# Performance work log

Measured on AMD Instinct MI355X. Metric: run time of the kernel, lower is better.

The kernel has to match this reference:

```python
import jax, jax.numpy as jnp
import numpy as np

N = 100000
E = 1600000
IN = 770
H = 64
R = 3

def _w(key, shape):
    fan_in = shape[-2] if len(shape) >= 2 else shape[-1]
    return jax.random.normal(key, shape, dtype=jnp.float32) / np.sqrt(fan_in)

def setup_inputs() -> dict:
    key = jax.random.key(0)
    ks = jax.random.split(key, 24)
    x = jax.random.normal(ks[0], (N, IN), dtype=jnp.float32)
    edge_index = jax.random.randint(ks[1], (2, E), 0, N, dtype=jnp.int64)
    edge_type = jax.random.randint(ks[2], (E,), 0, R, dtype=jnp.int64)
    return {
        "x": x, "edge_index": edge_index, "edge_type": edge_type,
        "W1": _w(ks[3], (R, IN, H)), "root1": _w(ks[4], (IN, H)), "b1": jnp.zeros((H,), jnp.float32),
        "W2": _w(ks[5], (R, H, H)), "root2": _w(ks[6], (H, H)), "b2": jnp.zeros((H,), jnp.float32),
        "W3": _w(ks[7], (R, H, H)), "root3": _w(ks[8], (H, H)), "b3": jnp.zeros((H,), jnp.float32),
        "nw1": _w(ks[9], (H, H // 2)), "nb1": jnp.zeros((H // 2,), jnp.float32),
        "nw2": _w(ks[10], (H // 2, 2)), "nb2": jnp.zeros((2,), jnp.float32),
        "ew1": _w(ks[11], (2 * H, H)), "eb1": jnp.zeros((H,), jnp.float32),
        "ew2": _w(ks[12], (H, H // 2)), "eb2": jnp.zeros((H // 2,), jnp.float32),
        "ew3": _w(ks[13], (H // 2, 3)), "eb3": jnp.zeros((3,), jnp.float32),
    }

def rgcn_layer(x, W, root, b, src, dst, etype):
    # PyG RGCNConv (aggr='mean'): out = x@root + b + sum_r mean_r(x_src)@W_r
    out = x @ root + b
    msg = x[src]                       # [E, F] gather
    for r in range(R):
        m = (etype == r).astype(x.dtype)
        agg = jax.ops.segment_sum(msg * m[:, None], dst, num_segments=N)  # [N, F]
        cnt = jax.ops.segment_sum(m, dst, num_segments=N)                 # [N]
        out = out + (agg / jnp.maximum(cnt, 1.0)[:, None]) @ W[r]
    return out

def reference(x, edge_index, edge_type,
              W1, root1, b1, W2, root2, b2, W3, root3, b3,
              nw1, nb1, nw2, nb2, ew1, eb1, ew2, eb2, ew3, eb3):
    src, dst = edge_index[0], edge_index[1]
    x1 = jax.nn.relu(rgcn_layer(x, W1, root1, b1, src, dst, edge_type))
    x2 = jax.nn.relu(rgcn_layer(x1, W2, root2, b2, src, dst, edge_type))
    x3 = rgcn_layer(x2, W3, root3, b3, src, dst, edge_type) + x1
    node_out = jax.nn.relu(x3 @ nw1 + nb1) @ nw2 + nb2
    ef = jnp.concatenate([x3[src], x3[dst]], axis=-1)   # [E, 2H]
    h = jax.nn.relu(ef @ ew1 + eb1)
    h = jax.nn.relu(h @ ew2 + eb2)
    edge_out = h @ ew3 + eb3
    return node_out, edge_out
```

## Files before the change

kernel.cpp:

```cpp
#include <hip/hip_runtime.h>

typedef unsigned int uint;
typedef unsigned short ushort;
typedef short short8 __attribute__((ext_vector_type(8)));
typedef float f32x4 __attribute__((ext_vector_type(4)));
typedef float float4u __attribute__((ext_vector_type(4), aligned(4)));

#define MN 100000
#define ME 1600000
#define KIN 770

__device__ __forceinline__ ushort f2bf(float f) {
    union { float f; uint u; } c; c.f = f;
    uint r = (c.u + 0x7fffu + ((c.u >> 16) & 1u)) >> 16;
    return (ushort)r;
}
__device__ __forceinline__ float bf2f(ushort h) {
    union { uint u; float f; } c; c.u = ((uint)h) << 16;
    return c.f;
}
__device__ __forceinline__ float bflo(uint w) {
    union { uint u; float f; } c; c.u = w << 16; return c.f;
}
__device__ __forceinline__ float bfhi(uint w) {
    union { uint u; float f; } c; c.u = w & 0xffff0000u; return c.f;
}

__global__ void k_deg(const int* __restrict__ dstv, int* __restrict__ deg, int E) {
    int e = blockIdx.x * blockDim.x + threadIdx.x;
    if (e < E) atomicAdd(&deg[dstv[e]], 1);
}

__global__ void k_scan1(const int* __restrict__ deg, int* __restrict__ excl,
                        int* __restrict__ csums, int n) {
    __shared__ int a[256], b[256];
    int tid = threadIdx.x;
    int g = blockIdx.x * 256 + tid;
    int v = (g < n) ? deg[g] : 0;
    int *cur = a, *nxt = b;
    cur[tid] = v;
    __syncthreads();
    for (int off = 1; off < 256; off <<= 1) {
        int t = cur[tid];
        if (tid >= off) t += cur[tid - off];
        nxt[tid] = t;
        __syncthreads();
        int* tmp = cur; cur = nxt; nxt = tmp;
    }
    int inc = cur[tid];
    if (g < n) excl[g] = inc - v;
    if (tid == 255) csums[blockIdx.x] = inc;
}

__global__ void k_scan2(int* __restrict__ csums, int nchunks) {
    __shared__ int a[512], b[512];
    int tid = threadIdx.x;
    int v = (tid < nchunks) ? csums[tid] : 0;
    int *cur = a, *nxt = b;
    cur[tid] = v;
    __syncthreads();
    for (int off = 1; off < 512; off <<= 1) {
        int t = cur[tid];
        if (tid >= off) t += cur[tid - off];
        nxt[tid] = t;
        __syncthreads();
        int* tmp = cur; cur = nxt; nxt = tmp;
    }
    int inc = cur[tid];
    if (tid < nchunks) csums[tid] = inc - v;
}

__global__ void k_scan3(int* __restrict__ row_ptr, const int* __restrict__ csums,
                        int* __restrict__ cursor, int n, int E) {
    int g = blockIdx.x * blockDim.x + threadIdx.x;
    if (g < n) {
        int v = row_ptr[g] + csums[g >> 8];
        row_ptr[g] = v;
        cursor[g] = v;
    }
    if (g == n) row_ptr[n] = E;
}

__global__ void k_fill(const int* __restrict__ srcv, const int* __restrict__ dstv,
                       const int* __restrict__ et, int* __restrict__ cursor,
                       int* __restrict__ esrt, int* __restrict__ dstp,
                       int* __restrict__ eid, int E) {
    int e = blockIdx.x * blockDim.x + threadIdx.x;
    if (e < E) {
        int d = dstv[e];
        int pos = atomicAdd(&cursor[d], 1);
        esrt[pos] = srcv[e] | (et[e] << 17);
        dstp[pos] = d;
        eid[pos] = e;
    }
}

__global__ void k_pack_bt(const float* __restrict__ root, const float* __restrict__ W,
                          ushort* __restrict__ out, int K, int Kp) {
    int idx = blockIdx.x * blockDim.x + threadIdx.x;
    if (idx >= 256 * Kp) return;
    int j = idx / Kp, k = idx - j * Kp;
    float v = 0.f;
    if (k < K) {
        if (j < 64) v = root[k * 64 + j];
        else {
            int r = (j >> 6) - 1, jj = j & 63;
            v = W[((size_t)r * K + k) * 64 + jj];
        }
    }
    out[idx] = f2bf(v);
}

__global__ void k_packwab_bt(const float* __restrict__ ew1, ushort* __restrict__ out) {
    int idx = blockIdx.x * blockDim.x + threadIdx.x;
    if (idx >= 128 * 64) return;
    int j = idx >> 6, k = idx & 63;
    float v = (j < 64) ? ew1[k * 64 + j] : ew1[(64 + k) * 64 + (j - 64)];
    out[idx] = f2bf(v);
}

template<bool AFP32, int BN>
__global__ __launch_bounds__(512) void k_mm(const void* __restrict__ Ain,
                                            const ushort* __restrict__ BT,
                                            ushort* __restrict__ C,
                                            int M, int K, int Kp, int Nc) {
    constexpr int WN = BN / 4;
    constexpr int NF = WN / 16;
    constexpr int NBS = (4 * BN) / 512;
    __shared__ uint4 lds4[512 + 4 * BN];
    int tid = threadIdx.x;
    int lane = tid & 63, wid = tid >> 6;
    int l15 = lane & 15, kq = lane >> 4;
    int wm = wid >> 2, wn = wid & 3;
    int m0 = blockIdx.x * 128;
    int n0 = blockIdx.y * BN;

    int s_kp = tid >> 7;
    int s_row = tid & 127;
    int gm = m0 + s_row; if (gm > M - 1) gm = M - 1;

    const float*  Af = (const float*)Ain;
    const ushort* Ab = (const ushort*)Ain;

    f32x4 acc[4][NF];
    #pragma unroll
    for (int m = 0; m < 4; ++m)
        #pragma unroll
        for (int n = 0; n < NF; ++n)
            acc[m][n] = (f32x4)0.f;

    int nkt = (K + 31) >> 5;
    uint4 stA, stB[NBS];

    auto loadA = [&](int kt) {
        int k0 = kt << 5;
        int kb = k0 + s_kp * 8;
        if constexpr (AFP32) {
            const float* ap = Af + (size_t)gm * K + kb;
            float v[8];
            if (k0 + 32 <= K) {
                *(float4u*)&v[0] = *(const float4u*)ap;
                *(float4u*)&v[4] = *(const float4u*)(ap + 4);
            } else {
                #pragma unroll
                for (int i = 0; i < 8; ++i)
                    v[i] = (kb + i < K) ? ap[i] : 0.f;
            }
            uint w[4];
            #pragma unroll
            for (int i = 0; i < 4; ++i)
                w[i] = (uint)f2bf(v[2 * i]) | ((uint)f2bf(v[2 * i + 1]) << 16);
            stA = make_uint4(w[0], w[1], w[2], w[3]);
        } else {
            stA = *(const uint4*)(Ab + (size_t)gm * K + kb);
        }
    };
    auto loadB = [&](int kt) {
        int k0 = kt << 5;
        #pragma unroll
        for (int is = 0; is < NBS; ++is) {
            int slot = is * 512 + tid;
            int kp = slot / BN;
            int col = slot & (BN - 1);
            stB[is] = *(const uint4*)(BT + (size_t)(n0 + col) * Kp + k0 + kp * 8);
        }
    };

    loadA(0); loadB(0);
    for (int kt = 0; kt < nkt; ++kt) {
        __syncthreads();
        lds4[tid] = stA;
        #pragma unroll
        for (int is = 0; is < NBS; ++is)
            lds4[512 + is * 512 + tid] = stB[is];
        __syncthreads();
        if (kt + 1 < nkt) { loadA(kt + 1); loadB(kt + 1); }
        const short8* Asv = (const short8*)lds4;
        const short8* Bsv = (const short8*)(lds4 + 512);
        short8 a[4], b[NF];
        #pragma unroll
        for (int m = 0; m < 4; ++m)
            a[m] = Asv[kq * 128 + wm * 64 + m * 16 + l15];
        #pragma unroll
        for (int n = 0; n < NF; ++n)
            b[n] = Bsv[kq * BN + wn * WN + n * 16 + l15];
        #pragma unroll
        for (int m = 0; m < 4; ++m)
            #pragma unroll
            for (int n = 0; n < NF; ++n)
                acc[m][n] = __builtin_amdgcn_mfma_f32_16x16x32_bf16(a[m], b[n], acc[m][n], 0, 0, 0);
    }

    #pragma unroll
    for (int m = 0; m < 4; ++m) {
        int rbase = m0 + wm * 64 + m * 16 + kq * 4;
        #pragma unroll
        for (int n = 0; n < NF; ++n) {
            int col = n0 + wn * WN + n * 16 + l15;
            #pragma unroll
            for (int rg = 0; rg < 4; ++rg) {
                int r = rbase + rg;
                if (r < M) C[(size_t)r * Nc + col] = f2bf(acc[m][n][rg]);
            }
        }
    }
}

__global__ __launch_bounds__(256) void k_agg(const ushort* __restrict__ Y,
                                             const int* __restrict__ row_ptr,
                                             const int* __restrict__ esrt,
                                             const float* __restrict__ bias,
                                             const ushort* __restrict__ resid,
                                             ushort* __restrict__ Xout,
                                             int do_relu, int n) {
    int wid = (blockIdx.x * blockDim.x + threadIdx.x) >> 6;
    int lane = threadIdx.x & 63;
    if (wid >= n) return;
    int beg = row_ptr[wid], end = row_ptr[wid + 1];
    float self = bf2f(Y[(size_t)wid * 256 + lane]);
    float bv = bias[lane];
    float a0 = 0.f, a1 = 0.f, a2 = 0.f;
    int c0 = 0, c1 = 0, c2 = 0;
    int e = beg;
    for (; e + 4 <= end; e += 4) {
        int p0 = esrt[e], p1 = esrt[e + 1], p2 = esrt[e + 2], p3 = esrt[e + 3];
        float v0 = bf2f(Y[(size_t)(p0 & 0x1FFFF) * 256 + 64 + ((p0 >> 17) << 6) + lane]);
        float v1 = bf2f(Y[(size_t)(p1 & 0x1FFFF) * 256 + 64 + ((p1 >> 17) << 6) + lane]);
        float v2 = bf2f(Y[(size_t)(p2 & 0x1FFFF) * 256 + 64 + ((p2 >> 17) << 6) + lane]);
        float v3 = bf2f(Y[(size_t)(p3 & 0x1FFFF) * 256 + 64 + ((p3 >> 17) << 6) + lane]);
        int r0 = p0 >> 17, r1 = p1 >> 17, r2 = p2 >> 17, r3 = p3 >> 17;
        if (r0 == 0) { a0 += v0; c0++; } else if (r0 == 1) { a1 += v0; c1++; } else { a2 += v0; c2++; }
        if (r1 == 0) { a0 += v1; c0++; } else if (r1 == 1) { a1 += v1; c1++; } else { a2 += v1; c2++; }
        if (r2 == 0) { a0 += v2; c0++; } else if (r2 == 1) { a1 += v2; c1++; } else { a2 += v2; c2++; }
        if (r3 == 0) { a0 += v3; c0++; } else if (r3 == 1) { a1 += v3; c1++; } else { a2 += v3; c2++; }
    }
    for (; e < end; ++e) {
        int p = esrt[e];
        int r = p >> 17;
        float v = bf2f(Y[(size_t)(p & 0x1FFFF) * 256 + 64 + (r << 6) + lane]);
        if (r == 0) { a0 += v; c0++; } else if (r == 1) { a1 += v; c1++; } else { a2 += v; c2++; }
    }
    float res = self + bv;
    if (c0) res += a0 / (float)c0;
    if (c1) res += a1 / (float)c1;
    if (c2) res += a2 / (float)c2;
    if (do_relu) res = fmaxf(res, 0.f);
    if (resid) res += bf2f(resid[(size_t)wid * 64 + lane]);
    Xout[(size_t)wid * 64 + lane] = f2bf(res);
}

__global__ __launch_bounds__(256) void k_nodehead(const ushort* __restrict__ X3,
                                                  const float* __restrict__ nw1,
                                                  const float* __restrict__ nb1,
                                                  const float* __restrict__ nw2,
                                                  const float* __restrict__ nb2,
                                                  float* __restrict__ out, int n) {
    __shared__ float w1[64 * 32];
    __shared__ float w2[32 * 2];
    __shared__ float b1s[32];
    __shared__ float b2s[2];
    int tid = threadIdx.x;
    for (int i = tid; i < 64 * 32; i += 256) w1[i] = nw1[i];
    for (int i = tid; i < 32 * 2; i += 256) w2[i] = nw2[i];
    if (tid < 32) b1s[tid] = nb1[tid];
    if (tid < 2) b2s[tid] = nb2[tid];
    __syncthreads();
    int g = blockIdx.x * blockDim.x + tid;
    if (g >= n) return;
    float x[64];
    const uint4* xr = (const uint4*)(X3 + (size_t)g * 64);
    #pragma unroll
    for (int q = 0; q < 8; ++q) {
        uint4 u = xr[q];
        x[q * 8 + 0] = bflo(u.x); x[q * 8 + 1] = bfhi(u.x);
        x[q * 8 + 2] = bflo(u.y); x[q * 8 + 3] = bfhi(u.y);
        x[q * 8 + 4] = bflo(u.z); x[q * 8 + 5] = bfhi(u.z);
        x[q * 8 + 6] = bflo(u.w); x[q * 8 + 7] = bfhi(u.w);
    }
    float o0 = b2s[0], o1 = b2s[1];
    for (int j = 0; j < 32; ++j) {
        float h = b1s[j];
        #pragma unroll
        for (int k = 0; k < 64; ++k) h += x[k] * w1[k * 32 + j];
        h = fmaxf(h, 0.f);
        o0 += h * w2[j * 2 + 0];
        o1 += h * w2[j * 2 + 1];
    }
    out[g * 2 + 0] = o0;
    out[g * 2 + 1] = o1;
}

__global__ __launch_bounds__(256) void k_edgehead(const ushort* __restrict__ AB,
                                                  const int* __restrict__ esrt,
                                                  const int* __restrict__ dstp,
                                                  const int* __restrict__ eid,
                                                  const float* __restrict__ eb1,
                                                  const float* __restrict__ ew2,
                                                  const float* __restrict__ eb2,
                                                  const float* __restrict__ ew3,
                                                  const float* __restrict__ eb3,
                                                  float* __restrict__ out, int E) {
    __shared__ float w2[64 * 32];
    __shared__ float w3[32 * 3];
    __shared__ float b1s[64];
    __shared__ float b2s[32];
    __shared__ float b3s[3];
    int tid = threadIdx.x;
    for (int i = tid; i < 64 * 32; i += 256) w2[i] = ew2[i];
    for (int i = tid; i < 32 * 3; i += 256) w3[i] = ew3[i];
    if (tid < 64) b1s[tid] = eb1[tid];
    if (tid < 32) b2s[tid] = eb2[tid];
    if (tid < 3) b3s[tid] = eb3[tid];
    __syncthreads();
    int p = blockIdx.x * blockDim.x + tid;
    if (p >= E) return;
    int s = esrt[p] & 0x1FFFF;
    int d = dstp[p];
    int e = eid[p];
    const uint4* Ar = (const uint4*)(AB + (size_t)s * 128);
    uint4 a4[8];
    #pragma unroll
    for (int q = 0; q < 8; ++q) a4[q] = Ar[q];
    const uint4* Br = (const uint4*)(AB + (size_t)d * 128 + 64);
    float h2[32];
    #pragma unroll
    for (int j = 0; j < 32; ++j) h2[j] = 0.f;
    #pragma unroll
    for (int q = 0; q < 8; ++q) {
        uint4 ua = a4[q], ub = Br[q];
        float af[8], bfv[8];
        af[0] = bflo(ua.x); af[1] = bfhi(ua.x); af[2] = bflo(ua.y); af[3] = bfhi(ua.y);
        af[4] = bflo(ua.z); af[5] = bfhi(ua.z); af[6] = bflo(ua.w); af[7] = bfhi(ua.w);
        bfv[0] = bflo(ub.x); bfv[1] = bfhi(ub.x); bfv[2] = bflo(ub.y); bfv[3] = bfhi(ub.y);
        bfv[4] = bflo(ub.z); bfv[5] = bfhi(ub.z); bfv[6] = bflo(ub.w); bfv[7] = bfhi(ub.w);
        #pragma unroll
        for (int t = 0; t < 8; ++t) {
            int k = q * 8 + t;
            float h1 = fmaxf(af[t] + bfv[t] + b1s[k], 0.f);
            #pragma unroll
            for (int j = 0; j < 32; ++j) h2[j] += h1 * w2[k * 32 + j];
        }
    }
    float o0 = b3s[0], o1 = b3s[1], o2 = b3s[2];
    #pragma unroll
    for (int j = 0; j < 32; ++j) {
        float hh = fmaxf(h2[j] + b2s[j], 0.f);
        o0 += hh * w3[j * 3 + 0];
        o1 += hh * w3[j * 3 + 1];
        o2 += hh * w3[j * 3 + 2];
    }
    out[200000 + (size_t)e * 3 + 0] = o0;
    out[200000 + (size_t)e * 3 + 1] = o1;
    out[200000 + (size_t)e * 3 + 2] = o2;
}

extern "C" void kernel_launch(void* const* d_in, const int* in_sizes, int n_in,
                              void* d_out, int out_size, void* d_ws, size_t ws_size,
                              hipStream_t stream) {
    const float* x     = (const float*)d_in[0];
    const int*   ei    = (const int*)d_in[1];
    const int*   et    = (const int*)d_in[2];
    const float* W1    = (const float*)d_in[3];
    const float* root1 = (const float*)d_in[4];
    const float* b1    = (const float*)d_in[5];
    const float* W2    = (const float*)d_in[6];
    const float* root2 = (const float*)d_in[7];
    const float* b2    = (const float*)d_in[8];
    const float* W3    = (const float*)d_in[9];
    const float* root3 = (const float*)d_in[10];
    const float* b3    = (const float*)d_in[11];
    const float* nw1   = (const float*)d_in[12];
    const float* nb1   = (const float*)d_in[13];
    const float* nw2   = (const float*)d_in[14];
    const float* nb2   = (const float*)d_in[15];
    const float* ew1   = (const float*)d_in[16];
    const float* eb1   = (const float*)d_in[17];
    const float* ew2   = (const float*)d_in[18];
    const float* eb2   = (const float*)d_in[19];
    const float* ew3   = (const float*)d_in[20];
    const float* eb3   = (const float*)d_in[21];
    float* out = (float*)d_out;

    const int N = MN, E = ME;
    const int* srcv = ei;
    const int* dstv = ei + E;

    char* w = (char*)d_ws;
    ushort* Yb   = (ushort*)w; w += (size_t)N * 256 * 2;
    ushort* X1b  = (ushort*)w; w += (size_t)N * 64 * 2;
    ushort* X2b  = (ushort*)w; w += (size_t)N * 64 * 2;
    ushort* X3b  = (ushort*)w; w += (size_t)N * 64 * 2;
    ushort* ABb  = (ushort*)w; w += (size_t)N * 128 * 2;
    ushort* BT1  = (ushort*)w; w += 256 * 800 * 2;
    ushort* BT2  = (ushort*)w; w += 256 * 64 * 2;
    ushort* BT3  = (ushort*)w; w += 256 * 64 * 2;
    ushort* BTab = (ushort*)w; w += 128 * 64 * 2;
    int* deg     = (int*)w; w += (size_t)N * 4;
    int* row_ptr = (int*)w; w += (size_t)(N + 1) * 4;
    int* cursor  = (int*)w; w += (size_t)N * 4;
    int* esrt    = (int*)w; w += (size_t)E * 4;
    int* dstp    = (int*)w; w += (size_t)E * 4;
    int* eid     = (int*)w; w += (size_t)E * 4;
    int* csums   = (int*)w; w += 512 * 4;

    hipMemsetAsync(deg, 0, N * sizeof(int), stream);
    k_deg<<<(E + 255) / 256, 256, 0, stream>>>(dstv, deg, E);
    int nchunks = (N + 255) / 256;
    k_scan1<<<nchunks, 256, 0, stream>>>(deg, row_ptr, csums, N);
    k_scan2<<<1, 512, 0, stream>>>(csums, nchunks);
    k_scan3<<<(N + 256) / 256, 256, 0, stream>>>(row_ptr, csums, cursor, N, E);
    k_fill<<<(E + 255) / 256, 256, 0, stream>>>(srcv, dstv, et, cursor, esrt, dstp, eid, E);

    k_pack_bt<<<(256 * 800 + 255) / 256, 256, 0, stream>>>(root1, W1, BT1, KIN, 800);
    k_pack_bt<<<(256 * 64 + 255) / 256, 256, 0, stream>>>(root2, W2, BT2, 64, 64);
    k_pack_bt<<<(256 * 64 + 255) / 256, 256, 0, stream>>>(root3, W3, BT3, 64, 64);
    k_packwab_bt<<<(128 * 64 + 255) / 256, 256, 0, stream>>>(ew1, BTab);

    int gx = (N + 127) / 128;
    int agg_grid = (N * 64 + 255) / 256;

    k_mm<true, 256><<<dim3(gx, 1), 512, 0, stream>>>(x, BT1, Yb, N, KIN, 800, 256);
    k_agg<<<agg_grid, 256, 0, stream>>>(Yb, row_ptr, esrt, b1, nullptr, X1b, 1, N);

    k_mm<false, 256><<<dim3(gx, 1), 512, 0, stream>>>(X1b, BT2, Yb, N, 64, 64, 256);
    k_agg<<<agg_grid, 256, 0, stream>>>(Yb, row_ptr, esrt, b2, nullptr, X2b, 1, N);

    k_mm<false, 256><<<dim3(gx, 1), 512, 0, stream>>>(X2b, BT3, Yb, N, 64, 64, 256);
    k_agg<<<agg_grid, 256, 0, stream>>>(Yb, row_ptr, esrt, b3, X1b, X3b, 0, N);

    k_nodehead<<<(N + 255) / 256, 256, 0, stream>>>(X3b, nw1, nb1, nw2, nb2, out, N);

    k_mm<false, 128><<<dim3(gx, 1), 512, 0, stream>>>(X3b, BTab, ABb, N, 64, 64, 128);
    k_edgehead<<<(E + 255) / 256, 256, 0, stream>>>(ABb, esrt, dstp, eid, eb1, ew2, eb2, ew3, eb3, out, E);
}
```

Before: 1.244 ms.

## Double K-tile depth to 64 and coalesce A/B staging loads in GEMM

The GEMM kernel now processes a K-tile of 64 instead of 32 per iteration, staging two MFMA K-halves per LDS fill and halving the number of barrier pairs. Global loads are remapped so eight consecutive threads read one row's 64-element K span contiguously, improving coalescing for the fp32 input and the B matrix. The fp32-to-bf16 conversion is deferred until the LDS store, so loads of the next tile can be issued before conversion. The cost is doubled LDS use and more staging registers, and the padded B layout for layer 1 grows to 832 columns.

```diff
diff --git a/kernel.cpp b/kernel.cpp
--- a/kernel.cpp
+++ b/kernel.cpp
@@ -126,18 +126,18 @@
                                             int M, int K, int Kp, int Nc) {
     constexpr int WN = BN / 4;
     constexpr int NF = WN / 16;
-    constexpr int NBS = (4 * BN) / 512;
-    __shared__ uint4 lds4[512 + 4 * BN];
+    constexpr int BR = BN / 64;
+    __shared__ uint4 lds4[1024 + 8 * BN];
     int tid = threadIdx.x;
     int lane = tid & 63, wid = tid >> 6;
-    int l15 = lane & 15, kq = lane >> 4;
+    int l15 = lane & 15, kqw = lane >> 4;
     int wm = wid >> 2, wn = wid & 3;
     int m0 = blockIdx.x * 128;
     int n0 = blockIdx.y * BN;
 
-    int s_kp = tid >> 7;
-    int s_row = tid & 127;
-    int gm = m0 + s_row; if (gm > M - 1) gm = M - 1;
+    int s_g = tid & 7;
+    int s_h = s_g >> 2, s_kq = s_g & 3;
+    int s_r = tid >> 3;
 
     const float*  Af = (const float*)Ain;
     const ushort* Ab = (const ushort*)Ain;
@@ -149,71 +149,85 @@
         for (int n = 0; n < NF; ++n)
             acc[m][n] = (f32x4)0.f;
 
-    int nkt = (K + 31) >> 5;
-    uint4 stA, stB[NBS];
+    int nkt = (K + 63) >> 6;
+    float stAf[2][8];
+    uint4 stAb[2];
+    uint4 stB[BR];
 
     auto loadA = [&](int kt) {
-        int k0 = kt << 5;
-        int kb = k0 + s_kp * 8;
-        if constexpr (AFP32) {
-            const float* ap = Af + (size_t)gm * K + kb;
-            float v[8];
-            if (k0 + 32 <= K) {
-                *(float4u*)&v[0] = *(const float4u*)ap;
-                *(float4u*)&v[4] = *(const float4u*)(ap + 4);
+        int k0 = kt << 6;
+        int kb = k0 + s_g * 8;
+        #pragma unroll
+        for (int r = 0; r < 2; ++r) {
+            int gm = m0 + s_r + (r << 6);
+            if (gm > M - 1) gm = M - 1;
+            if constexpr (AFP32) {
+                const float* ap = Af + (size_t)gm * K + kb;
+                if (k0 + 64 <= K) {
+                    *(float4u*)&stAf[r][0] = *(const float4u*)ap;
+                    *(float4u*)&stAf[r][4] = *(const float4u*)(ap + 4);
+                } else {
+                    #pragma unroll
+                    for (int i = 0; i < 8; ++i)
+                        stAf[r][i] = (kb + i < K) ? ap[i] : 0.f;
+                }
             } else {
-                #pragma unroll
-                for (int i = 0; i < 8; ++i)
-                    v[i] = (kb + i < K) ? ap[i] : 0.f;
+                stAb[r] = *(const uint4*)(Ab + (size_t)gm * K + kb);
             }
-            uint w[4];
-            #pragma unroll
-            for (int i = 0; i < 4; ++i)
-                w[i] = (uint)f2bf(v[2 * i]) | ((uint)f2bf(v[2 * i + 1]) << 16);
-            stA = make_uint4(w[0], w[1], w[2], w[3]);
-        } else {
-            stA = *(const uint4*)(Ab + (size_t)gm * K + kb);
         }
     };
     auto loadB = [&](int kt) {
-        int k0 = kt << 5;
-        #pragma unroll
-        for (int is = 0; is < NBS; ++is) {
-            int slot = is * 512 + tid;
-            int kp = slot / BN;
-            int col = slot & (BN - 1);
-            stB[is] = *(const uint4*)(BT + (size_t)(n0 + col) * Kp + k0 + kp * 8);
+        int k0 = kt << 6;
+        #pragma unroll
+        for (int r = 0; r < BR; ++r) {
+            int col = s_r + (r << 6);
+            stB[r] = *(const uint4*)(BT + (size_t)(n0 + col) * Kp + k0 + s_g * 8);
         }
     };
 
     loadA(0); loadB(0);
     for (int kt = 0; kt < nkt; ++kt) {
         __syncthreads();
-        lds4[tid] = stA;
-        #pragma unroll
-        for (int is = 0; is < NBS; ++is)
-            lds4[512 + is * 512 + tid] = stB[is];
+        #pragma unroll
+        for (int r = 0; r < 2; ++r) {
+            uint4 val;
+            if constexpr (AFP32) {
+                uint w0 = (uint)f2bf(stAf[r][0]) | ((uint)f2bf(stAf[r][1]) << 16);
+                uint w1 = (uint)f2bf(stAf[r][2]) | ((uint)f2bf(stAf[r][3]) << 16);
+                uint w2 = (uint)f2bf(stAf[r][4]) | ((uint)f2bf(stAf[r][5]) << 16);
+                uint w3 = (uint)f2bf(stAf[r][6]) | ((uint)f2bf(stAf[r][7]) << 16);
+                val = make_uint4(w0, w1, w2, w3);
+            } else {
+                val = stAb[r];
+            }
+            lds4[s_h * 512 + s_kq * 128 + s_r + (r << 6)] = val;
+        }
+        #pragma unroll
+        for (int r = 0; r < BR; ++r)
+            lds4[1024 + s_h * (4 * BN) + s_kq * BN + s_r + (r << 6)] = stB[r];
         __syncthreads();
         if (kt + 1 < nkt) { loadA(kt + 1); loadB(kt + 1); }
         const short8* Asv = (const short8*)lds4;
-        const short8* Bsv = (const short8*)(lds4 + 512);
-        short8 a[4], b[NF];
-        #pragma unroll
-        for (int m = 0; m < 4; ++m)
-            a[m] = Asv[kq * 128 + wm * 64 + m * 16 + l15];
-        #pragma unroll
-        for (int n = 0; n < NF; ++n)
-            b[n] = Bsv[kq * BN + wn * WN + n * 16 + l15];
-        #pragma unroll
-        for (int m = 0; m < 4; ++m)
+        #pragma unroll
+        for (int h = 0; h < 2; ++h) {
+            short8 a[4], b[NF];
+            #pragma unroll
+            for (int m = 0; m < 4; ++m)
+                a[m] = Asv[h * 512 + kqw * 128 + wm * 64 + m * 16 + l15];
             #pragma unroll
             for (int n = 0; n < NF; ++n)
-                acc[m][n] = __builtin_amdgcn_mfma_f32_16x16x32_bf16(a[m], b[n], acc[m][n], 0, 0, 0);
+                b[n] = Asv[1024 + h * (4 * BN) + kqw * BN + wn * WN + n * 16 + l15];
+            #pragma unroll
+            for (int m = 0; m < 4; ++m)
+                #pragma unroll
+                for (int n = 0; n < NF; ++n)
+                    acc[m][n] = __builtin_amdgcn_mfma_f32_16x16x32_bf16(a[m], b[n], acc[m][n], 0, 0, 0);
+        }
     }
 
     #pragma unroll
     for (int m = 0; m < 4; ++m) {
-        int rbase = m0 + wm * 64 + m * 16 + kq * 4;
+        int rbase = m0 + wm * 64 + m * 16 + kqw * 4;
         #pragma unroll
         for (int n = 0; n < NF; ++n) {
             int col = n0 + wn * WN + n * 16 + l15;
@@ -411,7 +425,7 @@
     ushort* X2b  = (ushort*)w; w += (size_t)N * 64 * 2;
     ushort* X3b  = (ushort*)w; w += (size_t)N * 64 * 2;
     ushort* ABb  = (ushort*)w; w += (size_t)N * 128 * 2;
-    ushort* BT1  = (ushort*)w; w += 256 * 800 * 2;
+    ushort* BT1  = (ushort*)w; w += 256 * 832 * 2;
     ushort* BT2  = (ushort*)w; w += 256 * 64 * 2;
     ushort* BT3  = (ushort*)w; w += 256 * 64 * 2;
     ushort* BTab = (ushort*)w; w += 128 * 64 * 2;
@@ -431,7 +445,7 @@
     k_scan3<<<(N + 256) / 256, 256, 0, stream>>>(row_ptr, csums, cursor, N, E);
     k_fill<<<(E + 255) / 256, 256, 0, stream>>>(srcv, dstv, et, cursor, esrt, dstp, eid, E);
 
-    k_pack_bt<<<(256 * 800 + 255) / 256, 256, 0, stream>>>(root1, W1, BT1, KIN, 800);
+    k_pack_bt<<<(256 * 832 + 255) / 256, 256, 0, stream>>>(root1, W1, BT1, KIN, 832);
     k_pack_bt<<<(256 * 64 + 255) / 256, 256, 0, stream>>>(root2, W2, BT2, 64, 64);
     k_pack_bt<<<(256 * 64 + 255) / 256, 256, 0, stream>>>(root3, W3, BT3, 64, 64);
     k_packwab_bt<<<(128 * 64 + 255) / 256, 256, 0, stream>>>(ew1, BTab);
@@ -439,7 +453,7 @@
     int gx = (N + 127) / 128;
     int agg_grid = (N * 64 + 255) / 256;
 
-    k_mm<true, 256><<<dim3(gx, 1), 512, 0, stream>>>(x, BT1, Yb, N, KIN, 800, 256);
+    k_mm<true, 256><<<dim3(gx, 1), 512, 0, stream>>>(x, BT1, Yb, N, KIN, 832, 256);
     k_agg<<<agg_grid, 256, 0, stream>>>(Yb, row_ptr, esrt, b1, nullptr, X1b, 1, N);
 
     k_mm<false, 256><<<dim3(gx, 1), 512, 0, stream>>>(X1b, BT2, Yb, N, 64, 64, 256);
```

Result: slower. 1.297 ms (+4.2%).

## Aggregate before transform in RGCN layers 2-3 and split edge-head projection buffers

Applied to the files above, without the earlier changes.

Layers 2 and 3 now aggregate the 64-wide node features per relation first (k_aggX), then run a single K=256 matmul against stacked root/W weights, with bias, relu and residual fused into the matmul epilogue. Before, the matmul produced a 256-wide Y and the gather read that. The gather per edge now touches a 64-wide row of X instead of a 64-slice of a 256-wide Y row, which is meant to cut scattered memory traffic and drop one intermediate write. The edge-head projections now write into two separate 64-wide buffers so each per-edge row is contiguous. The cost is two matmul launches instead of one and a new BN=64 matmul path in which some threads sit idle during the B load.

```diff
diff --git a/kernel.cpp b/kernel.cpp
--- a/kernel.cpp
+++ b/kernel.cpp
@@ -111,22 +111,40 @@
     out[idx] = f2bf(v);
 }
 
-__global__ void k_packwab_bt(const float* __restrict__ ew1, ushort* __restrict__ out) {
+__global__ void k_pack_stack(const float* __restrict__ root, const float* __restrict__ W,
+                             ushort* __restrict__ out) {
     int idx = blockIdx.x * blockDim.x + threadIdx.x;
-    if (idx >= 128 * 64) return;
+    if (idx >= 64 * 256) return;
+    int j = idx >> 8, k = idx & 255;
+    float v;
+    if (k < 64) v = root[k * 64 + j];
+    else {
+        int r = (k >> 6) - 1, kk = k & 63;
+        v = W[((size_t)r * 64 + kk) * 64 + j];
+    }
+    out[idx] = f2bf(v);
+}
+
+__global__ void k_packab(const float* __restrict__ ew1, ushort* __restrict__ BTa,
+                         ushort* __restrict__ BTb) {
+    int idx = blockIdx.x * blockDim.x + threadIdx.x;
+    if (idx >= 64 * 64) return;
     int j = idx >> 6, k = idx & 63;
-    float v = (j < 64) ? ew1[k * 64 + j] : ew1[(64 + k) * 64 + (j - 64)];
-    out[idx] = f2bf(v);
+    BTa[idx] = f2bf(ew1[k * 64 + j]);
+    BTb[idx] = f2bf(ew1[(64 + k) * 64 + j]);
 }
 
 template<bool AFP32, int BN>
 __global__ __launch_bounds__(512) void k_mm(const void* __restrict__ Ain,
                                             const ushort* __restrict__ BT,
                                             ushort* __restrict__ C,
-                                            int M, int K, int Kp, int Nc) {
+                                            int M, int K, int Kp, int Nc,
+                                            const float* __restrict__ bias,
+                                            const ushort* __restrict__ resid,
+                                            int do_relu) {
     constexpr int WN = BN / 4;
     constexpr int NF = WN / 16;
-    constexpr int NBS = (4 * BN) / 512;
+    constexpr int NBS = (4 * BN >= 512) ? (4 * BN) / 512 : 1;
     __shared__ uint4 lds4[512 + 4 * BN];
     int tid = threadIdx.x;
     int lane = tid & 63, wid = tid >> 6;
@@ -177,12 +195,20 @@
     };
     auto loadB = [&](int kt) {
         int k0 = kt << 5;
-        #pragma unroll
-        for (int is = 0; is < NBS; ++is) {
-            int slot = is * 512 + tid;
-            int kp = slot / BN;
-            int col = slot & (BN - 1);
-            stB[is] = *(const uint4*)(BT + (size_t)(n0 + col) * Kp + k0 + kp * 8);
+        if constexpr (BN >= 128) {
+            #pragma unroll
+            for (int is = 0; is < NBS; ++is) {
+                int slot = is * 512 + tid;
+                int kp = slot / BN;
+                int col = slot & (BN - 1);
+                stB[is] = *(const uint4*)(BT + (size_t)(n0 + col) * Kp + k0 + kp * 8);
+            }
+        } else {
+            if (tid < 4 * BN) {
+                int kp = tid / BN;
+                int col = tid & (BN - 1);
+                stB[0] = *(const uint4*)(BT + (size_t)(n0 + col) * Kp + k0 + kp * 8);
+            }
         }
     };
 
@@ -190,9 +216,13 @@
     for (int kt = 0; kt < nkt; ++kt) {
         __syncthreads();
         lds4[tid] = stA;
-        #pragma unroll
-        for (int is = 0; is < NBS; ++is)
-            lds4[512 + is * 512 + tid] = stB[is];
+        if constexpr (BN >= 128) {
+            #pragma unroll
+            for (int is = 0; is < NBS; ++is)
+                lds4[512 + is * 512 + tid] = stB[is];
+        } else {
+            if (tid < 4 * BN) lds4[512 + tid] = stB[0];
+        }
         __syncthreads();
         if (kt + 1 < nkt) { loadA(kt + 1); loadB(kt + 1); }
         const short8* Asv = (const short8*)lds4;
@@ -217,10 +247,16 @@
         #pragma unroll
         for (int n = 0; n < NF; ++n) {
             int col = n0 + wn * WN + n * 16 + l15;
+            float bv = bias ? bias[col] : 0.f;
             #pragma unroll
             for (int rg = 0; rg < 4; ++rg) {
                 int r = rbase + rg;
-                if (r < M) C[(size_t)r * Nc + col] = f2bf(acc[m][n][rg]);
+                if (r < M) {
+                    float v = acc[m][n][rg] + bv;
+                    if (do_relu) v = fmaxf(v, 0.f);
+                    if (resid) v += bf2f(resid[(size_t)r * Nc + col]);
+                    C[(size_t)r * Nc + col] = f2bf(v);
+                }
             }
         }
     }
@@ -230,9 +266,8 @@
                                              const int* __restrict__ row_ptr,
                                              const int* __restrict__ esrt,
                                              const float* __restrict__ bias,
-                                             const ushort* __restrict__ resid,
                                              ushort* __restrict__ Xout,
-                                             int do_relu, int n) {
+                                             int n) {
     int wid = (blockIdx.x * blockDim.x + threadIdx.x) >> 6;
     int lane = threadIdx.x & 63;
     if (wid >= n) return;
@@ -264,9 +299,45 @@
     if (c0) res += a0 / (float)c0;
     if (c1) res += a1 / (float)c1;
     if (c2) res += a2 / (float)c2;
-    if (do_relu) res = fmaxf(res, 0.f);
-    if (resid) res += bf2f(resid[(size_t)wid * 64 + lane]);
+    res = fmaxf(res, 0.f);
     Xout[(size_t)wid * 64 + lane] = f2bf(res);
+}
+
+__global__ __launch_bounds__(256) void k_aggX(const ushort* __restrict__ X,
+                                              const int* __restrict__ row_ptr,
+                                              const int* __restrict__ esrt,
+                                              ushort* __restrict__ Xagg, int n) {
+    int wid = (blockIdx.x * blockDim.x + threadIdx.x) >> 6;
+    int lane = threadIdx.x & 63;
+    if (wid >= n) return;
+    int beg = row_ptr[wid], end = row_ptr[wid + 1];
+    ushort self = X[(size_t)wid * 64 + lane];
+    float a0 = 0.f, a1 = 0.f, a2 = 0.f;
+    int c0 = 0, c1 = 0, c2 = 0;
+    int e = beg;
+    for (; e + 4 <= end; e += 4) {
+        int p0 = esrt[e], p1 = esrt[e + 1], p2 = esrt[e + 2], p3 = esrt[e + 3];
+        float v0 = bf2f(X[(size_t)(p0 & 0x1FFFF) * 64 + lane]);
+        float v1 = bf2f(X[(size_t)(p1 & 0x1FFFF) * 64 + lane]);
+        float v2 = bf2f(X[(size_t)(p2 & 0x1FFFF) * 64 + lane]);
+        float v3 = bf2f(X[(size_t)(p3 & 0x1FFFF) * 64 + lane]);
+        int r0 = p0 >> 17, r1 = p1 >> 17, r2 = p2 >> 17, r3 = p3 >> 17;
+        if (r0 == 0) { a0 += v0; c0++; } else if (r0 == 1) { a1 += v0; c1++; } else { a2 += v0; c2++; }
+        if (r1 == 0) { a0 += v1; c0++; } else if (r1 == 1) { a1 += v1; c1++; } else { a2 += v1; c2++; }
+        if (r2 == 0) { a0 += v2; c0++; } else if (r2 == 1) { a1 += v2; c1++; } else { a2 += v2; c2++; }
+        if (r3 == 0) { a0 += v3; c0++; } else if (r3 == 1) { a1 += v3; c1++; } else { a2 += v3; c2++; }
+    }
+    for (; e < end; ++e) {
+        int p = esrt[e];
+        int r = p >> 17;
+        float v = bf2f(X[(size_t)(p & 0x1FFFF) * 64 + lane]);
+        if (r == 0) { a0 += v; c0++; } else if (r == 1) { a1 += v; c1++; } else { a2 += v; c2++; }
+    }
+    size_t base = (size_t)wid * 256;
+    Xagg[base + lane] = self;
+    Xagg[base + 64 + lane]  = f2bf(c0 ? a0 / (float)c0 : 0.f);
+    Xagg[base + 128 + lane] = f2bf(c1 ? a1 / (float)c1 : 0.f);
+    Xagg[base + 192 + lane] = f2bf(c2 ? a2 / (float)c2 : 0.f);
 }
 
 __global__ __launch_bounds__(256) void k_nodehead(const ushort* __restrict__ X3,
@@ -310,7 +381,8 @@
     out[g * 2 + 1] = o1;
 }
 
-__global__ __launch_bounds__(256) void k_edgehead(const ushort* __restrict__ AB,
+__global__ __launch_bounds__(256) void k_edgehead(const ushort* __restrict__ Abuf,
+                                                  const ushort* __restrict__ Bbuf,
                                                   const int* __restrict__ esrt,
                                                   const int* __restrict__ dstp,
                                                   const int* __restrict__ eid,
@@ -337,11 +409,11 @@
     int s = esrt[p] & 0x1FFFF;
     int d = dstp[p];
     int e = eid[p];
-    const uint4* Ar = (const uint4*)(AB + (size_t)s * 128);
+    const uint4* Ar = (const uint4*)(Abuf + (size_t)s * 64);
     uint4 a4[8];
     #pragma unroll
     for (int q = 0; q < 8; ++q) a4[q] = Ar[q];
-    const uint4* Br = (const uint4*)(AB + (size_t)d * 128 + 64);
+    const uint4* Br = (const uint4*)(Bbuf + (size_t)d * 64);
     float h2[32];
     #pragma unroll
     for (int j = 0; j < 32; ++j) h2[j] = 0.f;
@@ -410,11 +482,11 @@
     ushort* X1b  = (ushort*)w; w += (size_t)N * 64 * 2;
     ushort* X2b  = (ushort*)w; w += (size_t)N * 64 * 2;
     ushort* X3b  = (ushort*)w; w += (size_t)N * 64 * 2;
-    ushort* ABb  = (ushort*)w; w += (size_t)N * 128 * 2;
     ushort* BT1  = (ushort*)w; w += 256 * 800 * 2;
-    ushort* BT2  = (ushort*)w; w += 256 * 64 * 2;
-    ushort* BT3  = (ushort*)w; w += 256 * 64 * 2;
-    ushort* BTab = (ushort*)w; w += 128 * 64 * 2;
+    ushort* BT2s = (ushort*)w; w += 64 * 256 * 2;
+    ushort* BT3s = (ushort*)w; w += 64 * 256 * 2;
+    ushort* BTa  = (ushort*)w; w += 64 * 64 * 2;
+    ushort* BTb  = (ushort*)w; w += 64 * 64 * 2;
     int* deg     = (int*)w; w += (size_t)N * 4;
     int* row_ptr = (int*)w; w += (size_t)(N + 1) * 4;
     int* cursor  = (int*)w; w += (size_t)N * 4;
@@ -423,6 +495,10 @@
     int* eid     = (int*)w; w += (size_t)E * 4;
     int* csums   = (int*)w; w += 512 * 4;
 
+    ushort* Xagg = Yb;
+    ushort* Abuf = Yb;
+    ushort* Bbuf = Yb + (size_t)N * 64;
+
     hipMemsetAsync(deg, 0, N * sizeof(int), stream);
     k_deg<<<(E + 255) / 256, 256, 0, stream>>>(dstv, deg, E);
     int nchunks = (N + 255) / 256;
@@ -432,24 +508,31 @@
     k_fill<<<(E + 255) / 256, 256, 0, stream>>>(srcv, dstv, et, cursor, esrt, dstp, eid, E);
 
     k_pack_bt<<<(256 * 800 + 255) / 256, 256, 0, stream>>>(root1, W1, BT1, KIN, 800);
-    k_pack_bt<<<(256 * 64 + 255) / 256, 256, 0, stream>>>(root2, W2, BT2, 64, 64);
-    k_pack_bt<<<(256 * 64 + 255) / 256, 256, 0, stream>>>(root3, W3, BT3, 64, 64);
-    k_packwab_bt<<<(128 * 64 + 255) / 256, 256, 0, stream>>>(ew1, BTab);
+    k_pack_stack<<<(64 * 256 + 255) / 256, 256, 0, stream>>>(root2, W2, BT2s);
+    k_pack_stack<<<(64 * 256 + 255) / 256, 256, 0, stream>>>(root3, W3, BT3s);
+    k_packab<<<(64 * 64 + 255) / 256, 256, 0, stream>>>(ew1, BTa, BTb);
 
     int gx = (N + 127) / 128;
     int agg_grid = (N * 64 + 255) / 256;
 
-    k_mm<true, 256><<<dim3(gx, 1), 512, 0, stream>>>(x, BT1, Yb, N, KIN, 800, 256);
-    k_agg<<<agg_grid, 256, 0, stream>>>(Yb, row_ptr, esrt, b1, nullptr, X1b, 1, N);
-
-    k_mm<false, 256><<<dim3(gx, 1), 512, 0, stream>>>(X1b, BT2, Yb, N, 64, 64, 256);
-    k_agg<<<agg_grid, 256, 0, stream>>>(Yb, row_ptr, esrt, b2, nullptr, X2b, 1, N);
-
-    k_mm<false, 256><<<dim3(gx, 1), 512, 0, stream>>>(X2b, BT3, Yb, N, 64, 64, 256);
-    k_agg<<<agg_grid, 256, 0, stream>>>(Yb, row_ptr, esrt, b3, X1b, X3b, 0, N);
+    k_mm<true, 256><<<dim3(gx, 1), 512, 0, stream>>>(x, BT1, Yb, N, KIN, 800, 256,
+                                                     nullptr, nullptr, 0);
+    k_agg<<<agg_grid, 256, 0, stream>>>(Yb, row_ptr, esrt, b1, X1b, N);
+
+    k_aggX<<<agg_grid, 256, 0, stream>>>(X1b, row_ptr, esrt, Xagg, N);
+    k_mm<false, 64><<<dim3(gx, 1), 512, 0, stream>>>(Xagg, BT2s, X2b, N, 256, 256, 64,
+                                                     b2, nullptr, 1);
+
+    k_aggX<<<agg_grid, 256, 0, stream>>>(X2b, row_ptr, esrt, Xagg, N);
+    k_mm<false, 64><<<dim3(gx, 1), 512, 0, stream>>>(Xagg, BT3s, X3b, N, 256, 256, 64,
+                                                     b3, X1b, 0);
 
     k_nodehead<<<(N + 255) / 256, 256, 0, stream>>>(X3b, nw1, nb1, nw2, nb2, out, N);
 
-    k_mm<false, 128><<<dim3(gx, 1), 512, 0, stream>>>(X3b, BTab, ABb, N, 64, 64, 128);
-    k_edgehead<<<(E + 255) / 256, 256, 0, stream>>>(ABb, esrt, dstp, eid, eb1, ew2, eb2, ew3, eb3, out, E);
-}
+    k_mm<false, 64><<<dim3(gx, 1), 512, 0, stream>>>(X3b, BTa, Abuf, N, 64, 64, 64,
+                                                     nullptr, nullptr, 0);
+    k_mm<false, 64><<<dim3(gx, 1), 512, 0, stream>>>(X3b, BTb, Bbuf, N, 64, 64, 64,
+                                                     nullptr, nullptr, 0);
+    k_edgehead<<<(E + 255) / 256, 256, 0, stream>>>(Abuf, Bbuf, esrt, dstp, eid,
+                                                    eb1, ew2, eb2, ew3, eb3, out, E);
+}
```

Measured after the change: 1.258 ms. Within noise of the previous version (+1.0%).
